# Kernel optimization log

Measured on AMD Instinct MI355X. Metric: run time of the kernel, lower is better.

The kernel has to match this reference:

```python
import jax, jax.numpy as jnp
import numpy as np
from jax import lax

S, T, B = 32, 32, 512          # src len, tgt len, batch
H, E, A = 1024, 256, 1024      # hidden, embed, attention dim
VS, VT = 64, 70                # source / target char vocab
START = 1                      # data.tar_l2i[start_token]


def _gru_cell(gi, h, W_hh, b_hh):
    """torch GRUCell math. gi = x @ W_ih.T + b_ih, shape (B, 3H)."""
    gh = h @ W_hh.T + b_hh
    ir, iz, in_ = jnp.split(gi, 3, axis=-1)
    hr, hz, hn = jnp.split(gh, 3, axis=-1)
    r = jax.nn.sigmoid(ir + hr)
    z = jax.nn.sigmoid(iz + hz)
    n = jnp.tanh(in_ + r * hn)
    return (1.0 - z) * n + z * h


def setup_inputs() -> dict:
    key = jax.random.key(0)
    ks = jax.random.split(key, 16)
    n = lambda k, shp: jax.random.normal(k, shp, dtype=jnp.float32) * 0.05
    return {
        "source": jax.random.randint(ks[0], (S, B), 0, VS),
        "target": jax.random.randint(ks[1], (T, B), 0, VT),
        "teacher_forcing": 1,
        "emb_src": n(ks[2], (VS, E)),
        "W_ih_enc": n(ks[3], (3 * H, E)),
        "W_hh_enc": n(ks[4], (3 * H, H)),
        "b_ih_enc": n(ks[5], (3 * H,)),
        "b_hh_enc": n(ks[6], (3 * H,)),
        "emb_tgt": n(ks[7], (VT, E)),
        "W_attn": n(ks[8], (2 * H, A)),
        "b_attn": n(ks[9], (A,)),
        "v_attn": n(ks[10], (A,)),
        "W_ih_dec": n(ks[11], (3 * H, H + E)),
        "W_hh_dec": n(ks[12], (3 * H, H)),
        "b_ih_dec": n(ks[13], (3 * H,)),
        "b_hh_dec": n(ks[14], (3 * H,)),
        "W_out": n(ks[15], (H, VT)),
        "b_out": jnp.zeros((VT,), jnp.float32),
    }


def reference(source, target, teacher_forcing, emb_src, W_ih_enc, W_hh_enc,
              b_ih_enc, b_hh_enc, emb_tgt, W_attn, b_attn, v_attn,
              W_ih_dec, W_hh_dec, b_ih_dec, b_hh_dec, W_out, b_out):
    tf = bool(teacher_forcing)

    # ---------------- Encoder: GRU over (S, B) ----------------
    x_emb = emb_src[source]                                   # (S, B, E)
    # precompute input-to-hidden GEMM for all timesteps (big fused GEMM)
    gi_all = jnp.einsum('sbe,ge->sbg', x_emb, W_ih_enc) + b_ih_enc  # (S, B, 3H)

    def enc_step(h, gi_t):
        h = _gru_cell(gi_t, h, W_hh_enc, b_hh_enc)
        return h, h

    h0 = jnp.zeros((B, H), x_emb.dtype)
    h_enc, enc_ops = lax.scan(enc_step, h0, gi_all)           # enc_ops: (S, B, H)

    # ---------------- Decoder loop (t = 1 .. T-1) ----------------
    def dec_step(carry, tgt_t):
        h, x = carry
        emb = emb_tgt[x]                                      # (B, E)
        hx = jnp.broadcast_to(h[None], (S, B, H))
        feat = jnp.concatenate([hx, enc_ops], axis=-1)        # (S, B, 2H)
        energy = jnp.tanh(jnp.einsum('sbf,fa->sba', feat, W_attn) + b_attn)
        scores = energy @ v_attn                              # (S, B)
        alpha = jax.nn.softmax(scores, axis=0)                # over source positions
        ctx = jnp.einsum('sb,sbh->bh', alpha, enc_ops)        # (B, H)
        gi = jnp.concatenate([ctx, emb], axis=-1) @ W_ih_dec.T + b_ih_dec
        h_new = _gru_cell(gi, h, W_hh_dec, b_hh_dec)
        logits = h_new @ W_out + b_out                        # (B, VT)
        x_next = tgt_t if tf else jnp.argmax(logits, axis=1)
        return (h_new, x_next), (logits, alpha.T)             # attn row: (B, S)

    (_, _), (dec_logits, attn) = lax.scan(dec_step, (h_enc, target[0]), target[1:])

    # outputs[0] is the one-hot start token (outputs[:, :, start]=1, rows 1.. overwritten)
    row0 = jnp.zeros((B, VT), dec_logits.dtype).at[:, START].set(1.0)
    outputs = jnp.concatenate([row0[None], dec_logits], axis=0)  # (T, B, VT)
    return outputs, attn                                         # attn: (T-1, B, S)
```

## Files before the change

### kernel.cpp

```cpp
#include <hip/hip_runtime.h>
#include <hip/hip_bf16.h>

typedef __bf16 bfx8 __attribute__((ext_vector_type(8)));
typedef __bf16 bfx4 __attribute__((ext_vector_type(4)));
typedef float f32x4 __attribute__((ext_vector_type(4)));

#define MFMA __builtin_amdgcn_mfma_f32_16x16x32_bf16


__device__ __attribute__((aligned(256))) float  g_h[512 * 1024];
__device__ __attribute__((aligned(256))) float  g_hpart[512 * 1024];
__device__ __attribute__((aligned(256))) __bf16 g_hb[2][512 * 1024];
__device__ __attribute__((aligned(256))) __bf16 g_Adec[512 * 1024];
__device__ __attribute__((aligned(256))) __bf16 g_enc_ops[(size_t)32 * 512 * 1024];
__device__ __attribute__((aligned(256))) __bf16 g_enc_part[(size_t)32 * 512 * 1024];
__device__ __attribute__((aligned(256))) __bf16 g_sWhhe[(size_t)3072 * 1024];
__device__ __attribute__((aligned(256))) __bf16 g_sWihe[(size_t)3072 * 256];
__device__ __attribute__((aligned(256))) __bf16 g_sWhhd[(size_t)3072 * 1024];
__device__ __attribute__((aligned(256))) __bf16 g_sWihd[(size_t)3072 * 1280];
__device__ __attribute__((aligned(256))) __bf16 g_sWattnA[(size_t)1024 * 1024];
__device__ __attribute__((aligned(256))) __bf16 g_sWattnB[(size_t)1024 * 1024];
__device__ __attribute__((aligned(256))) __bf16 g_sWout[(size_t)128 * 1024];
__device__ __attribute__((aligned(256))) __bf16 g_embs[64 * 256];
__device__ __attribute__((aligned(256))) __bf16 g_embt[96 * 256];
__device__ __attribute__((aligned(256))) float  g_tblS[64 * 3072];
__device__ __attribute__((aligned(256))) float  g_tblT[70 * 3072];
__device__ __attribute__((aligned(256))) int    g_xsel[512];

__device__ __forceinline__ float fast_tanh(float x) {
    float cx = fminf(fmaxf(x, -15.f), 15.f);
    float e = __expf(-2.f * cx);
    return (1.f - e) / (1.f + e);
}

__global__ void k_cvt(const float* __restrict__ src, __bf16* __restrict__ dst,
                      int n4)
{
    int i = blockIdx.x * 256 + threadIdx.x;
    if (i >= n4) return;
    float4 v = ((const float4*)src)[i];
    __bf16 o[4] = {(__bf16)v.x, (__bf16)v.y, (__bf16)v.z, (__bf16)v.w};
    *(ushort2*)(dst + 4 * i) = *(ushort2*)o;
    *(ushort2*)(dst + 4 * i + 2) = *(ushort2*)(o + 2);
}

__global__ void swz_rm(const float* __restrict__ W, __bf16* __restrict__ out,
                       int nK, int total)
{
    int gid = blockIdx.x * 256 + threadIdx.x;
    if (gid >= total) return;
    int F = gid >> 6, L = gid & 63;
    int t = F / nK, c = F - t * nK;
    int K = nK * 32;
    const float* s = W + (size_t)(t * 16 + (L & 15)) * K + c * 32 + (L >> 4) * 8;
    __bf16 o[8];
#pragma unroll
    for (int u = 0; u < 8; u++) o[u] = (__bf16)s[u];
    *(uint4*)(out + (size_t)gid * 8) = *(uint4*)o;
}

__global__ void swz_cm(const float* __restrict__ W, __bf16* __restrict__ out,
                       int nK, int ldsrc, int nguard, int total)
{
    int gid = blockIdx.x * 256 + threadIdx.x;
    if (gid >= total) return;
    int F = gid >> 6, L = gid & 63;
    int t = F / nK, c = F - t * nK;
    int n = t * 16 + (L & 15);
    int k = c * 32 + (L >> 4) * 8;
    __bf16 o[8];
#pragma unroll
    for (int u = 0; u < 8; u++)
        o[u] = (n < nguard) ? (__bf16)W[(size_t)(k + u) * ldsrc + n] : (__bf16)0.f;
    *(uint4*)(out + (size_t)gid * 8) = *(uint4*)o;
}

__global__ void k_init(float* __restrict__ out)
{
    int idx = blockIdx.x * 256 + threadIdx.x;
    if (idx < 512 * 1024) { g_h[idx] = 0.f; g_hb[0][idx] = (__bf16)0.f; }
    if (idx < 512 * 70) out[idx] = (idx % 70 == 1) ? 1.f : 0.f;
}

__global__ __launch_bounds__(256) void k_tbl(
    const __bf16* __restrict__ emb, const __bf16* __restrict__ sW,
    int nKtot, int cOff, int vguard, float* __restrict__ tbl)
{
    __shared__ __bf16 sA[32 * 256];
    const int tid = threadIdx.x;
    const int w = tid >> 6, lane = tid & 63;
    const int r15 = lane & 15, q = lane >> 4;
    const int bx = blockIdx.x, m0 = blockIdx.y * 32;

#pragma unroll
    for (int i = 0; i < 4; i++) {
        int lin = tid + i * 256;
        int r = lin >> 5, U = lin & 31;
        uint4 v = *(const uint4*)(emb + (size_t)(m0 + r) * 256 + U * 8);
        *(uint4*)(sA + (r * 32 + (U ^ (r & 7))) * 8) = v;
    }
    __syncthreads();

    const size_t tb = (size_t)(bx * 4 + w);
    const __bf16* wp = sW + (tb * nKtot + cOff) * 512 + lane * 8;
    const int xk = r15 & 7;
    const int ar0 = r15 * 256, ar1 = (16 + r15) * 256;

    f32x4 acc[2];
    acc[0] = (f32x4){0.f, 0.f, 0.f, 0.f};
    acc[1] = (f32x4){0.f, 0.f, 0.f, 0.f};
#pragma unroll
    for (int c = 0; c < 8; c++) {
        int us = ((c * 4 + q) ^ xk) * 8;
        bfx8 a0 = *(const bfx8*)(sA + ar0 + us);
        bfx8 a1 = *(const bfx8*)(sA + ar1 + us);
        bfx8 wv = *(const bfx8*)(wp + c * 512);
        acc[0] = MFMA(a0, wv, acc[0], 0, 0, 0);
        acc[1] = MFMA(a1, wv, acc[1], 0, 0, 0);
    }
    const int n = bx * 64 + w * 16 + r15;
#pragma unroll
    for (int ms = 0; ms < 2; ms++)
#pragma unroll
        for (int reg = 0; reg < 4; reg++) {
            int row = m0 + ms * 16 + q * 4 + reg;
            if (row < vguard)
                tbl[(size_t)row * 3072 + n] = acc[ms][reg];
        }
}

__global__ __launch_bounds__(512, 4) void k_encpart(
    const __bf16* __restrict__ Amat, const __bf16* __restrict__ sW,
    __bf16* __restrict__ Cout)
{
    __shared__ __bf16 sA[2][64 * 256];
    const int tid = threadIdx.x;
    const int w = tid >> 6, lane = tid & 63;
    const int r15 = lane & 15, q = lane >> 4;
    const int sw = (blockIdx.x & 7) * 128 + (blockIdx.x >> 3);
    const int nx = sw & 3;
    const int n0 = nx * 256, m0 = (sw >> 2) * 64;

    int sr[4], sv[4], so[4];
#pragma unroll
    for (int i = 0; i < 4; i++) {
        int lin = tid + i * 512;
        sr[i] = lin >> 5;
        sv[i] = lin & 31;
        so[i] = (sr[i] * 32 + (sv[i] ^ (sr[i] & 7))) * 8;
    }

    uint4 regs[4];
#pragma unroll
    for (int i = 0; i < 4; i++)
        regs[i] = *(const uint4*)(Amat + (size_t)(m0 + sr[i]) * 1024 + sv[i] * 8);
#pragma unroll
    for (int i = 0; i < 4; i++)
        *(uint4*)(&sA[0][so[i]]) = regs[i];
    __syncthreads();

    const int xk = r15 & 7;
    f32x4 acc[2][4];
#pragma unroll
    for (int nn = 0; nn < 2; nn++)
#pragma unroll
        for (int mf = 0; mf < 4; mf++) acc[nn][mf] = (f32x4){0.f, 0.f, 0.f, 0.f};

    const __bf16* wp0 = sW + ((size_t)(nx * 16 + w * 2) * 32) * 512 + lane * 8;
    const __bf16* wp1 = wp0 + 32 * 512;
    const int ar0 = r15 * 256;
    const int ar1 = (16 + r15) * 256;
    const int ar2 = (32 + r15) * 256;
    const int ar3 = (48 + r15) * 256;

    for (int kc = 0; kc < 4; kc++) {
        if (kc < 3) {
#pragma unroll
            for (int i = 0; i < 4; i++)
                regs[i] = *(const uint4*)(Amat + (size_t)(m0 + sr[i]) * 1024 +
                                          (kc + 1) * 256 + sv[i] * 8);
        }
        const __bf16* sAb = sA[kc & 1];
        const __bf16* wq0 = wp0 + kc * 8 * 512;
        const __bf16* wq1 = wp1 + kc * 8 * 512;
#pragma unroll
        for (int c = 0; c < 8; c++) {
            int us = ((c * 4 + q) ^ xk) * 8;
            bfx8 a0 = *(const bfx8*)(sAb + ar0 + us);
            bfx8 a1 = *(const bfx8*)(sAb + ar1 + us);
            bfx8 a2 = *(const bfx8*)(sAb + ar2 + us);
            bfx8 a3 = *(const bfx8*)(sAb + ar3 + us);
            bfx8 w0 = *(const bfx8*)(wq0 + c * 512);
            bfx8 w1 = *(const bfx8*)(wq1 + c * 512);
            acc[0][0] = MFMA(a0, w0, acc[0][0], 0, 0, 0);
            acc[0][1] = MFMA(a1, w0, acc[0][1], 0, 0, 0);
            acc[0][2] = MFMA(a2, w0, acc[0][2], 0, 0, 0);
            acc[0][3] = MFMA(a3, w0, acc[0][3], 0, 0, 0);
            acc[1][0] = MFMA(a0, w1, acc[1][0], 0, 0, 0);
            acc[1][1] = MFMA(a1, w1, acc[1][1], 0, 0, 0);
            acc[1][2] = MFMA(a2, w1, acc[1][2], 0, 0, 0);
            acc[1][3] = MFMA(a3, w1, acc[1][3], 0, 0, 0);
        }
        if (kc < 3) {
#pragma unroll
            for (int i = 0; i < 4; i++)
                *(uint4*)(&sA[(kc + 1) & 1][so[i]]) = regs[i];
            __syncthreads();
        }
    }

    __bf16* sC = sA[0];
#pragma unroll
    for (int nn = 0; nn < 2; nn++) {
        const int cl = (w * 2 + nn) * 16 + r15;
#pragma unroll
        for (int mf = 0; mf < 4; mf++) {
#pragma unroll
            for (int reg = 0; reg < 4; reg++) {
                int row = mf * 16 + q * 4 + reg;
                sC[row * 256 + cl] = (__bf16)acc[nn][mf][reg];
            }
        }
    }
    __syncthreads();
#pragma unroll
    for (int i = 0; i < 4; i++) {
        int lin = tid + i * 512;
        int row = lin >> 5, unit = lin & 31;
        *(uint4*)(Cout + (size_t)(m0 + row) * 1024 + n0 + unit * 8) =
            *(const uint4*)(sC + row * 256 + unit * 8);
    }
}

#define GH_BODY(ACC)                                              \
    {                                                             \
        int us = ((c * 4 + q) ^ xk) * 8;                          \
        bfx8 a0 = *(const bfx8*)(sA1 + br0 + us);                 \
        bfx8 a1 = *(const bfx8*)(sA1 + br1 + us);                 \
        bfx8 w0 = *(const bfx8*)(xp0 + c * 512);                  \
        bfx8 w1 = *(const bfx8*)(xp1 + c * 512);                  \
        bfx8 w2 = *(const bfx8*)(xp2 + c * 512);                  \
        ACC[0][0] = MFMA(a0, w0, ACC[0][0], 0, 0, 0);             \
        ACC[0][1] = MFMA(a1, w0, ACC[0][1], 0, 0, 0);             \
        ACC[1][0] = MFMA(a0, w1, ACC[1][0], 0, 0, 0);             \
        ACC[1][1] = MFMA(a1, w1, ACC[1][1], 0, 0, 0);             \
        ACC[2][0] = MFMA(a0, w2, ACC[2][0], 0, 0, 0);             \
        ACC[2][1] = MFMA(a1, w2, ACC[2][1], 0, 0, 0);             \
    }

#define GI_BODY(ACC)                                              \
    {                                                             \
        bfx8 a0 = *(const bfx8*)(A0 + c * 32);                    \
        bfx8 a1 = *(const bfx8*)(A1 + c * 32);                    \
        bfx8 w0 = *(const bfx8*)(wp0 + c * 512);                  \
        bfx8 w1 = *(const bfx8*)(wp1 + c * 512);                  \
        bfx8 w2 = *(const bfx8*)(wp2 + c * 512);                  \
        ACC[0][0] = MFMA(a0, w0, ACC[0][0], 0, 0, 0);             \
        ACC[0][1] = MFMA(a1, w0, ACC[0][1], 0, 0, 0);             \
        ACC[1][0] = MFMA(a0, w1, ACC[1][0], 0, 0, 0);             \
        ACC[1][1] = MFMA(a1, w1, ACC[1][1], 0, 0, 0);             \
        ACC[2][0] = MFMA(a0, w2, ACC[2][0], 0, 0, 0);             \
        ACC[2][1] = MFMA(a1, w2, ACC[2][1], 0, 0, 0);             \
    }

__global__ __launch_bounds__(256, 2) void gru_enc(
    const __bf16* __restrict__ hb_in, __bf16* __restrict__ hb_out,
    const float* __restrict__ b1, const float* __restrict__ b2,
    const int* __restrict__ src_t, int enc_t)
{
    __shared__ __align__(16) unsigned char smem[77824];
    __bf16* sA1 = (__bf16*)smem;
    float*  sGh = (float*)(smem + 65536);
    const int tid = threadIdx.x;
    const int w = tid >> 6, lane = tid & 63;
    const int r15 = lane & 15, q = lane >> 4;
    const int j0 = blockIdx.x * 32, m0 = blockIdx.y * 32;
    const int jsub = w & 1;

#pragma unroll
    for (int i = 0; i < 16; i++) {
        int lin = tid + i * 256;
        int r = lin >> 7, U = lin & 127;
        uint4 v = *(const uint4*)(hb_in + (size_t)(m0 + r) * 1024 + U * 8);
        *(uint4*)(sA1 + (r * 128 + (U ^ (r & 7))) * 8) = v;
    }
    __syncthreads();

    const size_t tb = (size_t)(blockIdx.x * 2 + jsub);
    const int xk = r15 & 7;
    f32x4 acc[3][2];
#pragma unroll
    for (int s = 0; s < 3; s++)
#pragma unroll
        for (int ms = 0; ms < 2; ms++) acc[s][ms] = (f32x4){0.f, 0.f, 0.f, 0.f};

    const __bf16* xp0 = g_sWhhe + (tb * 32) * 512 + lane * 8;
    const __bf16* xp1 = g_sWhhe + ((tb + 64) * 32) * 512 + lane * 8;
    const __bf16* xp2 = g_sWhhe + ((tb + 128) * 32) * 512 + lane * 8;
    const int br0 = r15 * 1024, br1 = (16 + r15) * 1024;
    const int cbeg = (w < 2) ? 0 : 16;
#pragma unroll 8
    for (int c = cbeg; c < cbeg + 16; c++) GH_BODY(acc)

    if (w >= 2) {
#pragma unroll
        for (int s = 0; s < 3; s++)
#pragma unroll
            for (int ms = 0; ms < 2; ms++)
#pragma unroll
                for (int reg = 0; reg < 4; reg++)
                    sGh[((s * 2 + jsub) * 32 + ms * 16 + q * 4 + reg) * 16 + r15] =
                        acc[s][ms][reg];
    }
    __syncthreads();
    if (w < 2) {
        const int jj = j0 + jsub * 16 + r15;
        const float bb1[3] = {b1[jj], b1[1024 + jj], b1[2048 + jj]};
        const float bb2[3] = {b2[jj], b2[1024 + jj], b2[2048 + jj]};
#pragma unroll
        for (int ms = 0; ms < 2; ms++) {
#pragma unroll
            for (int reg = 0; reg < 4; reg++) {
                int bl = ms * 16 + q * 4 + reg;
                int b_ = m0 + bl;
                int xv = src_t[b_];
                xv = (xv < 0) ? 0 : (xv > 63 ? 63 : xv);
                const float* tv = g_tblS + (size_t)xv * 3072 + jj;
                float gh0 = acc[0][ms][reg] + bb1[0] +
                            sGh[((0 * 2 + jsub) * 32 + bl) * 16 + r15];
                float gh1 = acc[1][ms][reg] + bb1[1] +
                            sGh[((1 * 2 + jsub) * 32 + bl) * 16 + r15];
                float gh2 = acc[2][ms][reg] + bb1[2] +
                            sGh[((2 * 2 + jsub) * 32 + bl) * 16 + r15];
                float gi0 = tv[0]    + bb2[0];
                float gi1 = tv[1024] + bb2[1];
                float gi2 = tv[2048] + bb2[2];
                float r = 1.f / (1.f + __expf(-(gi0 + gh0)));
                float z = 1.f / (1.f + __expf(-(gi1 + gh1)));
                float n = fast_tanh(gi2 + r * gh2);
                size_t off = (size_t)b_ * 1024 + jj;
                float hv = (1.f - z) * n + z * g_h[off];
                g_h[off] = hv;
                hb_out[off] = (__bf16)hv;
                g_enc_ops[(size_t)enc_t * 524288 + off] = (__bf16)hv;
            }
        }
    }
}

__global__ __launch_bounds__(256, 2) void gru_dec(
    const __bf16* __restrict__ hb_in, __bf16* __restrict__ hb_out,
    const float* __restrict__ b1, const float* __restrict__ b2)
{
    __shared__ __align__(16) unsigned char smem[77824];
    __bf16* sA1 = (__bf16*)smem;
    float*  sGi = (float*)(smem + 65536);
    const int tid = threadIdx.x;
    const int w = tid >> 6, lane = tid & 63;
    const int r15 = lane & 15, q = lane >> 4;
    const int j0 = blockIdx.x * 32, m0 = blockIdx.y * 32;
    const int jsub = w & 1;

#pragma unroll
    for (int i = 0; i < 16; i++) {
        int lin = tid + i * 256;
        int r = lin >> 7, U = lin & 127;
        uint4 v = *(const uint4*)(hb_in + (size_t)(m0 + r) * 1024 + U * 8);
        *(uint4*)(sA1 + (r * 128 + (U ^ (r & 7))) * 8) = v;
    }
    __syncthreads();

    const size_t tb = (size_t)(blockIdx.x * 2 + jsub);
    const int xk = r15 & 7;
    f32x4 acc[3][2];
#pragma unroll
    for (int s = 0; s < 3; s++)
#pragma unroll
        for (int ms = 0; ms < 2; ms++) acc[s][ms] = (f32x4){0.f, 0.f, 0.f, 0.f};

    if (w < 2) {
        const __bf16* xp0 = g_sWhhd + (tb * 32) * 512 + lane * 8;
        const __bf16* xp1 = g_sWhhd + ((tb + 64) * 32) * 512 + lane * 8;
        const __bf16* xp2 = g_sWhhd + ((tb + 128) * 32) * 512 + lane * 8;
        const int br0 = r15 * 1024, br1 = (16 + r15) * 1024;
#pragma unroll 8
        for (int c = 0; c < 32; c++) GH_BODY(acc)
    } else {
        const __bf16* A0 = g_Adec + (size_t)(m0 + r15) * 1024 + q * 8;
        const __bf16* A1 = A0 + 16 * 1024;
        const __bf16* wp0 = g_sWihd + (tb * 40) * 512 + lane * 8;
        const __bf16* wp1 = g_sWihd + ((tb + 64) * 40) * 512 + lane * 8;
        const __bf16* wp2 = g_sWihd + ((tb + 128) * 40) * 512 + lane * 8;
#pragma unroll 8
        for (int c = 0; c < 32; c++) GI_BODY(acc)
#pragma unroll
        for (int s = 0; s < 3; s++)
#pragma unroll
            for (int ms = 0; ms < 2; ms++)
#pragma unroll
                for (int reg = 0; reg < 4; reg++)
                    sGi[((s * 2 + jsub) * 32 + ms * 16 + q * 4 + reg) * 16 + r15] =
                        acc[s][ms][reg];
    }
    __syncthreads();
    if (w < 2) {
        const int jj = j0 + jsub * 16 + r15;
        const float bb1[3] = {b1[jj], b1[1024 + jj], b1[2048 + jj]};
        const float bb2[3] = {b2[jj], b2[1024 + jj], b2[2048 + jj]};
#pragma unroll
        for (int ms = 0; ms < 2; ms++) {
#pragma unroll
            for (int reg = 0; reg < 4; reg++) {
                int bl = ms * 16 + q * 4 + reg;
                int b_ = m0 + bl;
                const float* tv = g_tblT + (size_t)g_xsel[b_] * 3072 + jj;
                float gh0 = acc[0][ms][reg] + bb1[0];
                float gh1 = acc[1][ms][reg] + bb1[1];
                float gh2 = acc[2][ms][reg] + bb1[2];
                float gi0 = sGi[((0 * 2 + jsub) * 32 + bl) * 16 + r15] +
                            tv[0]    + bb2[0];
                float gi1 = sGi[((1 * 2 + jsub) * 32 + bl) * 16 + r15] +
                            tv[1024] + bb2[1];
                float gi2 = sGi[((2 * 2 + jsub) * 32 + bl) * 16 + r15] +
                            tv[2048] + bb2[2];
                float r = 1.f / (1.f + __expf(-(gi0 + gh0)));
                float z = 1.f / (1.f + __expf(-(gi1 + gh1)));
                float n = fast_tanh(gi2 + r * gh2);
                size_t off = (size_t)b_ * 1024 + jj;
                float hv = (1.f - z) * n + z * g_h[off];
                g_h[off] = hv;
                hb_out[off] = (__bf16)hv;
            }
        }
    }
}

__global__ __launch_bounds__(256) void k_hl(
    const __bf16* __restrict__ src, const float* __restrict__ battn,
    const float* __restrict__ bout, int lrow, float* __restrict__ outp)
{
    __shared__ __bf16 sA[32 * 1024];
    const int tid = threadIdx.x;
    const int w = tid >> 6, lane = tid & 63;
    const int r15 = lane & 15, q = lane >> 4;
    const int bx = blockIdx.x, m0 = blockIdx.y * 32;

#pragma unroll
    for (int i = 0; i < 16; i++) {
        int lin = tid + i * 256;
        int r = lin >> 7, U = lin & 127;
        uint4 v = *(const uint4*)(src + (size_t)(m0 + r) * 1024 + U * 8);
        *(uint4*)(sA + (r * 128 + (U ^ (r & 7))) * 8) = v;
    }
    __syncthreads();

    const __bf16* sW;
    int n;
    if (bx < 16) {
        sW = g_sWattnA;
        n = bx * 64 + w * 16 + r15;
    } else {
        if (lrow < 0) return;
        sW = g_sWout;
        n = (bx - 16) * 64 + w * 16 + r15;
    }
    const size_t tb = (size_t)((bx < 16 ? bx : bx - 16) * 4 + w);
    const __bf16* wp = sW + (tb * 32) * 512 + lane * 8;
    const int xk = r15 & 7;
    const int ar0 = r15 * 1024, ar1 = (16 + r15) * 1024;

    f32x4 acc[2];
    acc[0] = (f32x4){0.f, 0.f, 0.f, 0.f};
    acc[1] = (f32x4){0.f, 0.f, 0.f, 0.f};
#pragma unroll 8
    for (int c = 0; c < 32; c++) {
        int us = ((c * 4 + q) ^ xk) * 8;
        bfx8 a0 = *(const bfx8*)(sA + ar0 + us);
        bfx8 a1 = *(const bfx8*)(sA + ar1 + us);
        bfx8 wv = *(const bfx8*)(wp + c * 512);
        acc[0] = MFMA(a0, wv, acc[0], 0, 0, 0);
        acc[1] = MFMA(a1, wv, acc[1], 0, 0, 0);
    }

    if (bx < 16) {
        float bv = battn[n];
#pragma unroll
        for (int ms = 0; ms < 2; ms++)
#pragma unroll
            for (int reg = 0; reg < 4; reg++)
                g_hpart[(size_t)(m0 + ms * 16 + q * 4 + reg) * 1024 + n] =
                    acc[ms][reg] + bv;
    } else if (n < 70) {
        float bv = bout[n];
#pragma unroll
        for (int ms = 0; ms < 2; ms++)
#pragma unroll
            for (int reg = 0; reg < 4; reg++)
                outp[(size_t)lrow * 35840 +
                     (size_t)(m0 + ms * 16 + q * 4 + reg) * 70 + n] =
                    acc[ms][reg] + bv;
    }
}

__global__ __launch_bounds__(256) void k_attn(
    int j, const int* __restrict__ target, const int* __restrict__ tf,
    const float* __restrict__ v_attn, float* __restrict__ out)
{
    const int b = blockIdx.x, tid = threadIdx.x;
    const int lane = tid & 63, wave = tid >> 6;
    __shared__ float sc[32], sal[32];
    __shared__ int sx;
    if (wave == 0) {
        int xv;
        if (j == 0) xv = target[b];
        else if (*tf) xv = target[j * 512 + b];
        else {
            const float* row = out + (size_t)j * 35840 + b * 70;
            float bv = row[lane]; int bi = lane;
            if (lane < 6) {
                float v2 = row[lane + 64];
                if (v2 > bv) { bv = v2; bi = lane + 64; }
            }
#pragma unroll
            for (int off = 32; off; off >>= 1) {
                float ov = __shfl_down(bv, off);
                int   oi = __shfl_down(bi, off);
                if (ov > bv || (ov == bv && oi < bi)) { bv = ov; bi = oi; }
            }
            xv = bi;
        }
        if (lane == 0) sx = (xv < 0) ? 0 : (xv > 69 ? 69 : xv);
    }
    float hpv[16], vsv[16];
    {
        const float* hp = g_hpart + (size_t)b * 1024;
#pragma unroll
        for (int u = 0; u < 8; u++) {
            hpv[u]     = hp[lane * 8 + u];
            hpv[8 + u] = hp[512 + lane * 8 + u];
            vsv[u]     = v_attn[lane * 8 + u];
            vsv[8 + u] = v_attn[512 + lane * 8 + u];
        }
    }
    __syncthreads();
    if (tid == 0) g_xsel[b] = sx;
    for (int s = wave * 8; s < wave * 8 + 8; s++) {
        const __bf16* ep = g_enc_part + ((size_t)s * 512 + b) * 1024;
        bfx8 e0 = *(const bfx8*)(ep + lane * 8);
        bfx8 e1 = *(const bfx8*)(ep + 512 + lane * 8);
        float part = 0.f;
#pragma unroll
        for (int u = 0; u < 8; u++) {
            part += vsv[u]     * fast_tanh((float)e0[u] + hpv[u]);
            part += vsv[8 + u] * fast_tanh((float)e1[u] + hpv[8 + u]);
        }
#pragma unroll
        for (int off = 32; off; off >>= 1) part += __shfl_down(part, off);
        if (lane == 0) sc[s] = part;
    }
    __syncthreads();
    float mx = sc[0];
#pragma unroll
    for (int s = 1; s < 32; s++) mx = fmaxf(mx, sc[s]);
    float den = 0.f;
#pragma unroll
    for (int s = 0; s < 32; s++) den += __expf(sc[s] - mx);
    float rden = 1.f / den;
    if (tid < 32) {
        float al = __expf(sc[tid] - mx) * rden;
        sal[tid] = al;
        out[1146880 + (size_t)j * 16384 + b * 32 + tid] = al;
    }
    __syncthreads();
    float c0 = 0, c1 = 0, c2 = 0, c3 = 0;
    const __bf16* eo = g_enc_ops + (size_t)b * 1024 + tid * 4;
#pragma unroll 4
    for (int s = 0; s < 32; s++) {
        bfx4 e = *(const bfx4*)(eo + (size_t)s * 524288);
        float al = sal[s];
        c0 += al * (float)e[0]; c1 += al * (float)e[1];
        c2 += al * (float)e[2]; c3 += al * (float)e[3];
    }
    bfx4 o = {(__bf16)c0, (__bf16)c1, (__bf16)c2, (__bf16)c3};
    *(bfx4*)(&g_Adec[(size_t)b * 1024 + tid * 4]) = o;
}

extern "C" void kernel_launch(void* const* d_in, const int* in_sizes, int n_in,
                              void* d_out, int out_size, void* d_ws, size_t ws_size,
                              hipStream_t stream)
{
    const int*   source   = (const int*)d_in[0];
    const int*   target   = (const int*)d_in[1];
    const int*   tf       = (const int*)d_in[2];
    const float* emb_src  = (const float*)d_in[3];
    const float* W_ih_enc = (const float*)d_in[4];
    const float* W_hh_enc = (const float*)d_in[5];
    const float* b_ih_enc = (const float*)d_in[6];
    const float* b_hh_enc = (const float*)d_in[7];
    const float* emb_tgt  = (const float*)d_in[8];
    const float* W_attn   = (const float*)d_in[9];
    const float* b_attn   = (const float*)d_in[10];
    const float* v_attn   = (const float*)d_in[11];
    const float* W_ih_dec = (const float*)d_in[12];
    const float* W_hh_dec = (const float*)d_in[13];
    const float* b_ih_dec = (const float*)d_in[14];
    const float* b_hh_dec = (const float*)d_in[15];
    const float* W_out    = (const float*)d_in[16];
    const float* b_out    = (const float*)d_in[17];
    float* out = (float*)d_out;

    void *p_hb, *p_sWhhe, *p_sWihe, *p_sWhhd, *p_sWihd, *p_sWattnA, *p_sWattnB,
         *p_sWout, *p_embs, *p_embt, *p_enc_ops, *p_enc_part, *p_tblS, *p_tblT;
    hipGetSymbolAddress(&p_hb,       HIP_SYMBOL(g_hb));
    hipGetSymbolAddress(&p_sWhhe,    HIP_SYMBOL(g_sWhhe));
    hipGetSymbolAddress(&p_sWihe,    HIP_SYMBOL(g_sWihe));
    hipGetSymbolAddress(&p_sWhhd,    HIP_SYMBOL(g_sWhhd));
    hipGetSymbolAddress(&p_sWihd,    HIP_SYMBOL(g_sWihd));
    hipGetSymbolAddress(&p_sWattnA,  HIP_SYMBOL(g_sWattnA));
    hipGetSymbolAddress(&p_sWattnB,  HIP_SYMBOL(g_sWattnB));
    hipGetSymbolAddress(&p_sWout,    HIP_SYMBOL(g_sWout));
    hipGetSymbolAddress(&p_embs,     HIP_SYMBOL(g_embs));
    hipGetSymbolAddress(&p_embt,     HIP_SYMBOL(g_embt));
    hipGetSymbolAddress(&p_enc_ops,  HIP_SYMBOL(g_enc_ops));
    hipGetSymbolAddress(&p_enc_part, HIP_SYMBOL(g_enc_part));
    hipGetSymbolAddress(&p_tblS,     HIP_SYMBOL(g_tblS));
    hipGetSymbolAddress(&p_tblT,     HIP_SYMBOL(g_tblT));
    __bf16* hb0 = (__bf16*)p_hb;
    __bf16* hb1 = hb0 + 512 * 1024;

    k_cvt<<<16, 256, 0, stream>>>(emb_src, (__bf16*)p_embs, 64 * 256 / 4);
    k_cvt<<<18, 256, 0, stream>>>(emb_tgt, (__bf16*)p_embt, 70 * 256 / 4);
    swz_rm<<<1536, 256, 0, stream>>>(W_hh_enc, (__bf16*)p_sWhhe, 32, 393216);
    swz_rm<<<384,  256, 0, stream>>>(W_ih_enc, (__bf16*)p_sWihe, 8,  98304);
    swz_rm<<<1536, 256, 0, stream>>>(W_hh_dec, (__bf16*)p_sWhhd, 32, 393216);
    swz_rm<<<1920, 256, 0, stream>>>(W_ih_dec, (__bf16*)p_sWihd, 40, 491520);
    swz_cm<<<512,  256, 0, stream>>>(W_attn, (__bf16*)p_sWattnA, 32, 1024, 1024, 131072);
    swz_cm<<<512,  256, 0, stream>>>(W_attn + (size_t)1024 * 1024,
                                     (__bf16*)p_sWattnB, 32, 1024, 1024, 131072);
    swz_cm<<<64,   256, 0, stream>>>(W_out,  (__bf16*)p_sWout,   32, 70,   70,   16384);
    k_tbl<<<dim3(48, 2), 256, 0, stream>>>(
        (__bf16*)p_embs, (__bf16*)p_sWihe, 8,  0,  64, (float*)p_tblS);
    k_tbl<<<dim3(48, 3), 256, 0, stream>>>(
        (__bf16*)p_embt, (__bf16*)p_sWihd, 40, 32, 70, (float*)p_tblT);
    k_init<<<2048, 256, 0, stream>>>(out);

    for (int t = 0; t < 32; t++) {
        __bf16* hin  = (t & 1) ? hb1 : hb0;
        __bf16* hout = (t & 1) ? hb0 : hb1;
        gru_enc<<<dim3(32, 16), 256, 0, stream>>>(
            hin, hout, b_hh_enc, b_ih_enc, source + t * 512, t);
    }

    k_encpart<<<dim3(1024), 512, 0, stream>>>(
        (__bf16*)p_enc_ops, (__bf16*)p_sWattnB, (__bf16*)p_enc_part);

    k_hl<<<dim3(18, 16), 256, 0, stream>>>(hb0, b_attn, b_out, -1, out);

    for (int j = 0; j < 31; j++) {
        __bf16* hin  = (j & 1) ? hb1 : hb0;
        __bf16* hout = (j & 1) ? hb0 : hb1;
        k_attn<<<512, 256, 0, stream>>>(j, target, tf, v_attn, out);
        gru_dec<<<dim3(32, 16), 256, 0, stream>>>(hin, hout, b_hh_dec, b_ih_dec);
        k_hl<<<dim3(18, 16), 256, 0, stream>>>(hout, b_attn, b_out, j + 1, out);
    }
}
```

Before: 2.087 ms.

## Store bf16 hidden state in MFMA fragment layout and read directly from global

The GRU kernels now write the bf16 hidden state in a pre-tiled MFMA fragment order (hfrag_off), so the encoder, decoder and k_hl kernels can load A-operand fragments straight from global memory with coalesced 16-byte loads. The LDS staging of the 32x1024 hidden tile, its swizzle and the barrier are removed, which cuts LDS use from about 76KB to 12KB per block. This should raise occupancy and drop staging latency. The cost is that the same h fragments are re-read from global/L2 by every wave instead of once per block. Any other consumer of hb (e.g. the attention or k_hl inputs when not fed by these kernels) must also expect the new layout.

```diff
diff --git a/kernel.cpp b/kernel.cpp
--- a/kernel.cpp
+++ b/kernel.cpp
@@ -232,11 +232,10 @@
     }
 }
 
-#define GH_BODY(ACC)                                              \
+#define GH_BODY_G(ACC)                                            \
     {                                                             \
-        int us = ((c * 4 + q) ^ xk) * 8;                          \
-        bfx8 a0 = *(const bfx8*)(sA1 + br0 + us);                 \
-        bfx8 a1 = *(const bfx8*)(sA1 + br1 + us);                 \
+        bfx8 a0 = *(const bfx8*)(H0 + c * 512);                   \
+        bfx8 a1 = *(const bfx8*)(H1 + c * 512);                   \
         bfx8 w0 = *(const bfx8*)(xp0 + c * 512);                  \
         bfx8 w1 = *(const bfx8*)(xp1 + c * 512);                  \
         bfx8 w2 = *(const bfx8*)(xp2 + c * 512);                  \
@@ -263,44 +262,38 @@
         ACC[2][1] = MFMA(a1, w2, ACC[2][1], 0, 0, 0);             \
     }
 
+__device__ __forceinline__ size_t hfrag_off(int b, int jj) {
+    return ((size_t)(b >> 4) * 32 + (jj >> 5)) * 512 +
+           (size_t)(((b & 15) + 16 * ((jj & 31) >> 3)) * 8 + (jj & 7));
+}
+
 __global__ __launch_bounds__(256, 2) void gru_enc(
     const __bf16* __restrict__ hb_in, __bf16* __restrict__ hb_out,
     const float* __restrict__ b1, const float* __restrict__ b2,
     const int* __restrict__ src_t, int enc_t)
 {
-    __shared__ __align__(16) unsigned char smem[77824];
-    __bf16* sA1 = (__bf16*)smem;
-    float*  sGh = (float*)(smem + 65536);
+    __shared__ __align__(16) float sGh[3072];
     const int tid = threadIdx.x;
     const int w = tid >> 6, lane = tid & 63;
     const int r15 = lane & 15, q = lane >> 4;
     const int j0 = blockIdx.x * 32, m0 = blockIdx.y * 32;
     const int jsub = w & 1;
 
-#pragma unroll
-    for (int i = 0; i < 16; i++) {
-        int lin = tid + i * 256;
-        int r = lin >> 7, U = lin & 127;
-        uint4 v = *(const uint4*)(hb_in + (size_t)(m0 + r) * 1024 + U * 8);
-        *(uint4*)(sA1 + (r * 128 + (U ^ (r & 7))) * 8) = v;
-    }
-    __syncthreads();
-
     const size_t tb = (size_t)(blockIdx.x * 2 + jsub);
-    const int xk = r15 & 7;
     f32x4 acc[3][2];
 #pragma unroll
     for (int s = 0; s < 3; s++)
 #pragma unroll
         for (int ms = 0; ms < 2; ms++) acc[s][ms] = (f32x4){0.f, 0.f, 0.f, 0.f};
 
+    const __bf16* H0 = hb_in + (size_t)m0 * 1024 + lane * 8;
+    const __bf16* H1 = H0 + 16384;
     const __bf16* xp0 = g_sWhhe + (tb * 32) * 512 + lane * 8;
     const __bf16* xp1 = g_sWhhe + ((tb + 64) * 32) * 512 + lane * 8;
     const __bf16* xp2 = g_sWhhe + ((tb + 128) * 32) * 512 + lane * 8;
-    const int br0 = r15 * 1024, br1 = (16 + r15) * 1024;
     const int cbeg = (w < 2) ? 0 : 16;
 #pragma unroll 8
-    for (int c = cbeg; c < cbeg + 16; c++) GH_BODY(acc)
+    for (int c = cbeg; c < cbeg + 16; c++) GH_BODY_G(acc)
 
     if (w >= 2) {
 #pragma unroll
@@ -341,7 +334,7 @@
                 size_t off = (size_t)b_ * 1024 + jj;
                 float hv = (1.f - z) * n + z * g_h[off];
                 g_h[off] = hv;
-                hb_out[off] = (__bf16)hv;
+                hb_out[hfrag_off(b_, jj)] = (__bf16)hv;
                 g_enc_ops[(size_t)enc_t * 524288 + off] = (__bf16)hv;
             }
         }
@@ -352,26 +345,14 @@
     const __bf16* __restrict__ hb_in, __bf16* __restrict__ hb_out,
     const float* __restrict__ b1, const float* __restrict__ b2)
 {
-    __shared__ __align__(16) unsigned char smem[77824];
-    __bf16* sA1 = (__bf16*)smem;
-    float*  sGi = (float*)(smem + 65536);
+    __shared__ __align__(16) float sGi[3072];
     const int tid = threadIdx.x;
     const int w = tid >> 6, lane = tid & 63;
     const int r15 = lane & 15, q = lane >> 4;
     const int j0 = blockIdx.x * 32, m0 = blockIdx.y * 32;
     const int jsub = w & 1;
 
-#pragma unroll
-    for (int i = 0; i < 16; i++) {
-        int lin = tid + i * 256;
-        int r = lin >> 7, U = lin & 127;
-        uint4 v = *(const uint4*)(hb_in + (size_t)(m0 + r) * 1024 + U * 8);
-        *(uint4*)(sA1 + (r * 128 + (U ^ (r & 7))) * 8) = v;
-    }
-    __syncthreads();
-
     const size_t tb = (size_t)(blockIdx.x * 2 + jsub);
-    const int xk = r15 & 7;
     f32x4 acc[3][2];
 #pragma unroll
     for (int s = 0; s < 3; s++)
@@ -379,12 +360,13 @@
         for (int ms = 0; ms < 2; ms++) acc[s][ms] = (f32x4){0.f, 0.f, 0.f, 0.f};
 
     if (w < 2) {
+        const __bf16* H0 = hb_in + (size_t)m0 * 1024 + lane * 8;
+        const __bf16* H1 = H0 + 16384;
         const __bf16* xp0 = g_sWhhd + (tb * 32) * 512 + lane * 8;
         const __bf16* xp1 = g_sWhhd + ((tb + 64) * 32) * 512 + lane * 8;
         const __bf16* xp2 = g_sWhhd + ((tb + 128) * 32) * 512 + lane * 8;
-        const int br0 = r15 * 1024, br1 = (16 + r15) * 1024;
 #pragma unroll 8
-        for (int c = 0; c < 32; c++) GH_BODY(acc)
+        for (int c = 0; c < 32; c++) GH_BODY_G(acc)
     } else {
         const __bf16* A0 = g_Adec + (size_t)(m0 + r15) * 1024 + q * 8;
         const __bf16* A1 = A0 + 16 * 1024;
@@ -429,7 +411,7 @@
                 size_t off = (size_t)b_ * 1024 + jj;
                 float hv = (1.f - z) * n + z * g_h[off];
                 g_h[off] = hv;
-                hb_out[off] = (__bf16)hv;
+                hb_out[hfrag_off(b_, jj)] = (__bf16)hv;
             }
         }
     }
@@ -439,20 +421,10 @@
     const __bf16* __restrict__ src, const float* __restrict__ battn,
     const float* __restrict__ bout, int lrow, float* __restrict__ outp)
 {
-    __shared__ __bf16 sA[32 * 1024];
     const int tid = threadIdx.x;
     const int w = tid >> 6, lane = tid & 63;
     const int r15 = lane & 15, q = lane >> 4;
     const int bx = blockIdx.x, m0 = blockIdx.y * 32;
-
-#pragma unroll
-    for (int i = 0; i < 16; i++) {
-        int lin = tid + i * 256;
-        int r = lin >> 7, U = lin & 127;
-        uint4 v = *(const uint4*)(src + (size_t)(m0 + r) * 1024 + U * 8);
-        *(uint4*)(sA + (r * 128 + (U ^ (r & 7))) * 8) = v;
-    }
-    __syncthreads();
 
     const __bf16* sW;
     int n;
@@ -466,17 +438,16 @@
     }
     const size_t tb = (size_t)((bx < 16 ? bx : bx - 16) * 4 + w);
     const __bf16* wp = sW + (tb * 32) * 512 + lane * 8;
-    const int xk = r15 & 7;
-    const int ar0 = r15 * 1024, ar1 = (16 + r15) * 1024;
+    const __bf16* H0 = src + (size_t)m0 * 1024 + lane * 8;
+    const __bf16* H1 = H0 + 16384;
 
     f32x4 acc[2];
     acc[0] = (f32x4){0.f, 0.f, 0.f, 0.f};
     acc[1] = (f32x4){0.f, 0.f, 0.f, 0.f};
 #pragma unroll 8
     for (int c = 0; c < 32; c++) {
-        int us = ((c * 4 + q) ^ xk) * 8;
-        bfx8 a0 = *(const bfx8*)(sA + ar0 + us);
-        bfx8 a1 = *(const bfx8*)(sA + ar1 + us);
+        bfx8 a0 = *(const bfx8*)(H0 + c * 512);
+        bfx8 a1 = *(const bfx8*)(H1 + c * 512);
         bfx8 wv = *(const bfx8*)(wp + c * 512);
         acc[0] = MFMA(a0, wv, acc[0], 0, 0, 0);
         acc[1] = MFMA(a1, wv, acc[1], 0, 0, 0);
```

Result: slower. 2.304 ms (+10.4%).
